# Performance work log

Hardware: AMD Instinct MI355X
Metric: run time of the kernel (lower is better)

The kernel has to match this reference:

```python
import jax, jax.numpy as jnp
import numpy as np

B, N, DEG = 8, 4096, 16
E = N * DEG            # edges per graph
IN, HID, C, OUT = 128, 512, 2, 10
EPS = 1e-15


def setup_inputs() -> dict:
    key = jax.random.key(0)
    ks = jax.random.split(key, 16)
    # within-graph random edges, then offset each graph by b*N
    src = jax.random.randint(ks[0], (B, E), 0, N)
    dst = jax.random.randint(ks[1], (B, E), 0, N)
    off = (jnp.arange(B) * N)[:, None]
    edge_index = jnp.stack([(src + off).reshape(-1), (dst + off).reshape(-1)], axis=0).astype(jnp.int64)
    batch = jnp.repeat(jnp.arange(B), N).astype(jnp.int64)
    x = jax.random.normal(ks[2], (B * N, IN), dtype=jnp.float32)
    edge_weight = jax.random.uniform(ks[3], (B * E,), dtype=jnp.float32)
    g = lambda k, s: (0.02 * jax.random.normal(k, s, dtype=jnp.float32))
    return {
        "x": x, "edge_index": edge_index, "batch": batch, "edge_weight": edge_weight,
        "W_rel1": g(ks[4], (IN, HID)), "b_rel1": jnp.zeros((HID,), jnp.float32),
        "W_root1": g(ks[5], (IN, HID)),
        "W_pool": g(ks[6], (HID, C)), "b_pool": jnp.zeros((C,), jnp.float32),
        "W_rel3": g(ks[7], (HID, HID)), "b_rel3": jnp.zeros((HID,), jnp.float32),
        "W_root3": g(ks[8], (HID, HID)),
        "W_lin1": g(ks[9], (HID, HID)), "b_lin1": jnp.zeros((HID,), jnp.float32),
        "W_lin2": g(ks[10], (HID, OUT)), "b_lin2": jnp.zeros((OUT,), jnp.float32),
    }


def reference(x, edge_index, batch, edge_weight,
              W_rel1, b_rel1, W_root1, W_pool, b_pool,
              W_rel3, b_rel3, W_root3, W_lin1, b_lin1, W_lin2, b_lin2):
    src, dst = edge_index[0], edge_index[1]
    # GraphConv (aggr='add'): out = lin_rel(sum_j w_ji x_j) + lin_root(x)
    agg = jax.ops.segment_sum(x[src] * edge_weight[:, None], dst, num_segments=B * N)
    h = jax.nn.relu(agg @ W_rel1 + b_rel1 + x @ W_root1)          # [BN, HID]
    s_logits = h @ W_pool + b_pool                                 # [BN, C]

    # dense batched tensors (equal-size graphs)
    hd = h.reshape(B, N, HID)
    s = jax.nn.softmax(s_logits.reshape(B, N, C), axis=-1)
    b_idx = batch[src]
    r = src - b_idx * N
    c = dst - b_idx * N
    adj = jnp.zeros((B, N, N), jnp.float32).at[b_idx, r, c].add(edge_weight)

    # dense mincut pooling
    out = jnp.einsum('bnc,bnf->bcf', s, hd)                        # [B, C, HID]
    sA = jnp.einsum('bnc,bnm->bcm', s, adj)
    out_adj = jnp.einsum('bcm,bmk->bck', sA, s)                    # [B, C, C]
    mincut_num = jnp.einsum('bcc->b', out_adj)
    d = adj.sum(-1)                                                # [B, N]
    mincut_den = jnp.einsum('bnc,bn,bnc->b', s, d, s)
    mc_loss = jnp.mean(-(mincut_num / mincut_den))
    ss = jnp.einsum('bnc,bnk->bck', s, s)
    ss_n = ss / jnp.linalg.norm(ss, axis=(1, 2), keepdims=True)
    i_s = jnp.eye(C, dtype=jnp.float32) / jnp.sqrt(jnp.float32(C))
    o_loss = jnp.mean(jnp.linalg.norm(ss_n - i_s[None], axis=(1, 2)))
    # zero diagonal + symmetric degree normalization
    out_adj = out_adj * (1.0 - jnp.eye(C, dtype=jnp.float32))[None]
    d2 = jnp.sqrt(out_adj.sum(-1)) + EPS                           # [B, C]
    out_adj = out_adj / d2[:, :, None] / d2[:, None, :]

    # conv3 on pooled graph: edges (row->col) of dense adj => agg = A^T x
    agg3 = jnp.einsum('bij,bif->bjf', out_adj, out)
    x3 = agg3 @ W_rel3 + b_rel3 + out @ W_root3                    # [B, C, HID]
    xm = x3.mean(axis=1)                                           # [B, HID]
    h2 = jax.nn.relu(xm @ W_lin1 + b_lin1)
    logits = h2 @ W_lin2 + b_lin2
    return (jax.nn.log_softmax(logits, axis=-1), mc_loss, o_loss, s_logits, out_adj)
```

## Files before the change

### kernel.cpp

```cpp
#include <hip/hip_runtime.h>
#include <hip/hip_bf16.h>

#define BB 8
#define NN 4096
#define EE 65536
#define BE (BB*EE)
#define BN (BB*NN)
#define INF 128
#define HID 512
#define CC 2
#define OUTC 10
#define ELLCAP 64

typedef __bf16 bf16x8_t __attribute__((ext_vector_type(8)));
typedef float  f32x4_t  __attribute__((ext_vector_type(4)));

__device__ __forceinline__ ushort f2bf(float f) {
  union { float f; unsigned u; } v; v.f = f;
  unsigned r = v.u + 0x7FFFu + ((v.u >> 16) & 1u);
  return (ushort)(r >> 16);
}
__device__ __forceinline__ float bf2f(ushort s) {
  union { unsigned u; float f; } v; v.u = ((unsigned)s) << 16;
  return v.f;
}

__global__ __launch_bounds__(256) void front(
    const int* __restrict__ src, const int* __restrict__ dst,
    const float* __restrict__ ew, const float* __restrict__ x,
    const float* __restrict__ Wrel, const float* __restrict__ Wroot,
    int* __restrict__ deg, int2* __restrict__ ell,
    ushort* __restrict__ Ab, ushort* __restrict__ Bb) {
  int blk = blockIdx.x;
  int tid = threadIdx.x;
  if (blk < 4096) {
    int g = (blk & 7) * 131072 + (blk >> 3) * 256 + tid;
    float4 v = *(const float4*)&x[(size_t)g * 4];
    int m = g >> 5;
    int kin = (g & 31) * 4;
    ushort4 o;
    o.x = f2bf(v.x); o.y = f2bf(v.y); o.z = f2bf(v.z); o.w = f2bf(v.w);
    *(ushort4*)&Ab[(size_t)m * 256 + 128 + kin] = o;
  } else if (blk < 6144) {
    int bl = blk - 4096;
    int e = (bl & 7) * EE + (bl >> 3) * 256 + tid;
    int d = dst[e];
    int p = atomicAdd(&deg[d], 1);
    if (p < ELLCAP) {
      int2 v; v.x = src[e]; v.y = __float_as_int(ew[e]);
      ell[(size_t)d * ELLCAP + p] = v;
    }
  } else {
    int g = (blk - 6144) * 256 + tid;
    int n = g & 511, k = g >> 9;
    float w = (k < 128) ? Wrel[k * 512 + n] : Wroot[(k - 128) * 512 + n];
    Bb[n * 256 + k] = f2bf(w);
  }
}

__global__ __launch_bounds__(256) void gather_ell(
    const int* __restrict__ deg, const int2* __restrict__ ell,
    ushort* __restrict__ Ab) {
  int blk = blockIdx.x;
  int n = (blk & 7) * NN + (blk >> 3) * 4 + (threadIdx.x >> 6);
  int lane = threadIdx.x & 63;
  int l4 = lane >> 4;
  int fl = lane & 15;
  int d = deg[n]; if (d > ELLCAP) d = ELLCAP;
  const int2* ep = ell + (size_t)n * ELLCAP;

  float a[8] = {0, 0, 0, 0, 0, 0, 0, 0};
  int j = 0;
  for (; j + 7 < d; j += 8) {
    int2 v0 = ep[j + l4];
    int2 v1 = ep[j + 4 + l4];
    uint4 u0 = *(const uint4*)&Ab[(size_t)v0.x * 256 + 128 + fl * 8];
    uint4 u1 = *(const uint4*)&Ab[(size_t)v1.x * 256 + 128 + fl * 8];
    float w0 = __int_as_float(v0.y);
    float w1 = __int_as_float(v1.y);
    const ushort* s0 = (const ushort*)&u0;
    const ushort* s1 = (const ushort*)&u1;
#pragma unroll
    for (int q = 0; q < 8; ++q)
      a[q] += w0 * bf2f(s0[q]) + w1 * bf2f(s1[q]);
  }
  for (; j + 3 < d; j += 4) {
    int2 v0 = ep[j + l4];
    uint4 u0 = *(const uint4*)&Ab[(size_t)v0.x * 256 + 128 + fl * 8];
    float w0 = __int_as_float(v0.y);
    const ushort* s0 = (const ushort*)&u0;
#pragma unroll
    for (int q = 0; q < 8; ++q)
      a[q] += w0 * bf2f(s0[q]);
  }
  {
    int idx = j + l4;
    if (idx < d) {
      int2 v0 = ep[idx];
      uint4 u0 = *(const uint4*)&Ab[(size_t)v0.x * 256 + 128 + fl * 8];
      float w0 = __int_as_float(v0.y);
      const ushort* s0 = (const ushort*)&u0;
#pragma unroll
      for (int q = 0; q < 8; ++q)
        a[q] += w0 * bf2f(s0[q]);
    }
  }
#pragma unroll
  for (int q = 0; q < 8; ++q) {
    a[q] += __shfl_xor(a[q], 16, 64);
    a[q] += __shfl_xor(a[q], 32, 64);
  }
  if (l4 == 0) {
    ushort o[8];
#pragma unroll
    for (int q = 0; q < 8; ++q) o[q] = f2bf(a[q]);
    *(uint4*)&Ab[(size_t)n * 256 + fl * 8] = *(const uint4*)o;
  }
}

#define CPAD 72
__global__ __launch_bounds__(256) void gemm_mfma(
    const ushort* __restrict__ Ab, const ushort* __restrict__ Bb,
    const float* __restrict__ brel, ushort* __restrict__ hw) {
  __shared__ ushort As[64 * 256];
  __shared__ ushort Bs[64 * 256];
  int tid = threadIdx.x;
  int blk = blockIdx.x;
  int xcd = blk & 7;
  int idx = blk >> 3;
  int by = xcd * 64 + (idx & 63);
  int bx = idx >> 6;
  int m0 = by * 64, n0 = bx * 64;

#pragma unroll
  for (int i = 0; i < 8; ++i) {
    int g = tid + i * 256;
    int r = g >> 5, c = g & 31;
    int cs = c ^ (r & 31);
    *(uint4*)&As[(r * 32 + cs) * 8] = *(const uint4*)&Ab[(size_t)(m0 + r) * 256 + c * 8];
    *(uint4*)&Bs[(r * 32 + cs) * 8] = *(const uint4*)&Bb[(size_t)(n0 + r) * 256 + c * 8];
  }
  __syncthreads();

  int wave = tid >> 6, lane = tid & 63;
  int wm = (wave >> 1) * 32, wn = (wave & 1) * 32;
  int l16 = lane & 15, quad = lane >> 4;

  f32x4_t acc[2][2];
#pragma unroll
  for (int f = 0; f < 2; ++f)
#pragma unroll
    for (int g = 0; g < 2; ++g) acc[f][g] = (f32x4_t){0.f, 0.f, 0.f, 0.f};

  int arow[2] = {wm + l16, wm + 16 + l16};
  int brow[2] = {wn + l16, wn + 16 + l16};

#pragma unroll
  for (int kc = 0; kc < 8; ++kc) {
    int cl = kc * 4 + quad;
    bf16x8_t af[2], bf[2];
#pragma unroll
    for (int f = 0; f < 2; ++f) {
      af[f] = *(const bf16x8_t*)&As[(arow[f] * 32 + (cl ^ (arow[f] & 31))) * 8];
      bf[f] = *(const bf16x8_t*)&Bs[(brow[f] * 32 + (cl ^ (brow[f] & 31))) * 8];
    }
#pragma unroll
    for (int f = 0; f < 2; ++f)
#pragma unroll
      for (int g = 0; g < 2; ++g)
        acc[f][g] = __builtin_amdgcn_mfma_f32_16x16x32_bf16(af[f], bf[g], acc[f][g], 0, 0, 0);
  }
  __syncthreads();

  ushort* Cs = As;
#pragma unroll
  for (int g = 0; g < 2; ++g) {
    int col = wn + g * 16 + l16;
    float bias = brel[n0 + col];
#pragma unroll
    for (int f = 0; f < 2; ++f) {
      int rowb = wm + f * 16 + quad * 4;
#pragma unroll
      for (int r = 0; r < 4; ++r) {
        float v = fmaxf(acc[f][g][r] + bias, 0.f);
        Cs[(rowb + r) * CPAD + col] = f2bf(v);
      }
    }
  }
  __syncthreads();
  {
    int r = tid >> 2, co = (tid & 3) * 16;
    uint4 v0 = *(uint4*)&Cs[r * CPAD + co];
    uint4 v1 = *(uint4*)&Cs[r * CPAD + co + 8];
    *(uint4*)&hw[(size_t)(m0 + r) * 512 + n0 + co] = v0;
    *(uint4*)&hw[(size_t)(m0 + r) * 512 + n0 + co + 8] = v1;
  }
}

__global__ __launch_bounds__(256) void pool_node(
    const ushort* __restrict__ hw, const float* __restrict__ Wp,
    const float* __restrict__ bp, float* __restrict__ s,
    float* __restrict__ slog, float* __restrict__ outpart,
    float* __restrict__ ssacc) {
  __shared__ float red[4][1024];
  __shared__ float ssr[4][3];
  int blk = blockIdx.x;
  int b = blk & 7;
  int chunk = blk >> 3;
  int obik = b * 64 + chunk;
  int wave = threadIdx.x >> 6, lane = threadIdx.x & 63;
  int n0 = b * NN + chunk * 64 + wave * 16;
  int f0 = lane * 8;

  float wp0[8], wp1[8];
#pragma unroll
  for (int j = 0; j < 8; ++j) {
    wp0[j] = Wp[(f0 + j) * 2];
    wp1[j] = Wp[(f0 + j) * 2 + 1];
  }
  float bp0 = bp[0], bp1 = bp[1];
  float o0[8] = {0, 0, 0, 0, 0, 0, 0, 0};
  float o1[8] = {0, 0, 0, 0, 0, 0, 0, 0};
  float sa = 0.f, sb = 0.f, sc2 = 0.f;

  for (int i = 0; i < 16; ++i) {
    int n = n0 + i;
    bf16x8_t hv = *(const bf16x8_t*)&hw[(size_t)n * HID + f0];
    const ushort* hp = (const ushort*)&hv;
    float h[8];
    float a0 = 0.f, a1 = 0.f;
#pragma unroll
    for (int j = 0; j < 8; ++j) {
      h[j] = bf2f(hp[j]);
      a0 += h[j] * wp0[j];
      a1 += h[j] * wp1[j];
    }
#pragma unroll
    for (int off = 32; off; off >>= 1) {
      a0 += __shfl_down(a0, off, 64);
      a1 += __shfl_down(a1, off, 64);
    }
    float s0 = 0.f, s1 = 0.f;
    if (lane == 0) {
      float l0 = a0 + bp0, l1 = a1 + bp1;
      slog[n * 2] = l0;
      slog[n * 2 + 1] = l1;
      float m = fmaxf(l0, l1);
      float e0 = expf(l0 - m), e1 = expf(l1 - m);
      float inv = 1.f / (e0 + e1);
      s0 = e0 * inv; s1 = e1 * inv;
      s[n * 2] = s0;
      s[n * 2 + 1] = s1;
      sa += s0 * s0; sb += s0 * s1; sc2 += s1 * s1;
    }
    s0 = __shfl(s0, 0, 64);
    s1 = __shfl(s1, 0, 64);
#pragma unroll
    for (int j = 0; j < 8; ++j) {
      o0[j] += s0 * h[j];
      o1[j] += s1 * h[j];
    }
  }

#pragma unroll
  for (int j = 0; j < 8; ++j) {
    red[wave][f0 + j] = o0[j];
    red[wave][512 + f0 + j] = o1[j];
  }
  if (lane == 0) { ssr[wave][0] = sa; ssr[wave][1] = sb; ssr[wave][2] = sc2; }
  __syncthreads();
  int t = threadIdx.x;
#pragma unroll
  for (int q = 0; q < 4; ++q) {
    int idx = t + q * 256;
    float v = red[0][idx] + red[1][idx] + red[2][idx] + red[3][idx];
    outpart[(size_t)obik * 1024 + idx] = v;
  }
  if (t < 3) {
    float v = ssr[0][t] + ssr[1][t] + ssr[2][t] + ssr[3][t];
    atomicAdd(&ssacc[b * 4 + t], v);
  }
}

__global__ __launch_bounds__(256) void edge_pass2(
    const int* __restrict__ src, const int* __restrict__ dst,
    const float* __restrict__ ew, const float* __restrict__ s,
    float* __restrict__ oadj, float* __restrict__ mden) {
  int b = blockIdx.x & 7;
  int sub = blockIdx.x >> 3;
  int base = b * EE + sub * 1024;
  float p00 = 0, p01 = 0, p10 = 0, p11 = 0, md = 0;
  for (int i = threadIdx.x; i < 1024; i += 256) {
    int e = base + i;
    int r = src[e], c = dst[e];
    float w = ew[e];
    float s0r = s[r * 2], s1r = s[r * 2 + 1];
    float s0c = s[c * 2], s1c = s[c * 2 + 1];
    p00 += w * s0r * s0c; p01 += w * s0r * s1c;
    p10 += w * s1r * s0c; p11 += w * s1r * s1c;
    md  += w * (s0r * s0r + s1r * s1r);
  }
#pragma unroll
  for (int off = 32; off; off >>= 1) {
    p00 += __shfl_down(p00, off, 64);
    p01 += __shfl_down(p01, off, 64);
    p10 += __shfl_down(p10, off, 64);
    p11 += __shfl_down(p11, off, 64);
    md  += __shfl_down(md,  off, 64);
  }
  __shared__ float red[4][5];
  int wave = threadIdx.x >> 6, lane = threadIdx.x & 63;
  if (lane == 0) {
    red[wave][0] = p00; red[wave][1] = p01;
    red[wave][2] = p10; red[wave][3] = p11;
    red[wave][4] = md;
  }
  __syncthreads();
  if (threadIdx.x < 4) {
    float v = red[0][threadIdx.x] + red[1][threadIdx.x] +
              red[2][threadIdx.x] + red[3][threadIdx.x];
    atomicAdd(&oadj[b * 4 + threadIdx.x], v);
  } else if (threadIdx.x == 4) {
    float v = red[0][4] + red[1][4] + red[2][4] + red[3][4];
    atomicAdd(&mden[b], v);
  }
}

__global__ __launch_bounds__(256) void finalize_a(
    const float* __restrict__ outpart, const float* __restrict__ oadj,
    const float* __restrict__ ssacc, const float* __restrict__ mden,
    float* __restrict__ uv, float* __restrict__ lossp,
    float* __restrict__ dout) {
  __shared__ float sc[2];
  int b = blockIdx.x, t = threadIdx.x;
  if (t == 0) {
    float r00 = oadj[b * 4 + 0], r01 = oadj[b * 4 + 1];
    float r10 = oadj[b * 4 + 2], r11 = oadj[b * 4 + 3];
    lossp[b * 2 + 0] = -((r00 + r11) / mden[b]) / (float)BB;
    float a = ssacc[b * 4 + 0], bb = ssacc[b * 4 + 1], c = ssacc[b * 4 + 2];
    float nrm = sqrtf(a * a + 2.f * bb * bb + c * c);
    float q = 0.70710678118654752f;
    float da = a / nrm - q, db = bb / nrm, dc = c / nrm - q;
    lossp[b * 2 + 1] = sqrtf(da * da + 2.f * db * db + dc * dc) / (float)BB;
    float d20 = sqrtf(r01) + 1e-15f;
    float d21 = sqrtf(r10) + 1e-15f;
    float oa01 = r01 / (d20 * d21);
    float oa10 = r10 / (d21 * d20);
    dout[65618 + b * 4 + 0] = 0.f;
    dout[65618 + b * 4 + 1] = oa01;
    dout[65618 + b * 4 + 2] = oa10;
    dout[65618 + b * 4 + 3] = 0.f;
    sc[0] = oa01; sc[1] = oa10;
  }
  __syncthreads();
  float oa01 = sc[0], oa10 = sc[1];
  for (int f = t; f < HID; f += 256) {
    float o0 = 0.f, o1 = 0.f;
    for (int i = 0; i < 64; ++i) {
      o0 += outpart[(size_t)(b * 64 + i) * 1024 + f];
      o1 += outpart[(size_t)(b * 64 + i) * 1024 + 512 + f];
    }
    uv[b * HID + f] = oa10 * o1 + oa01 * o0;
    uv[BB * HID + b * HID + f] = o0 + o1;
  }
}

__global__ __launch_bounds__(256) void conv3_part(
    const float* __restrict__ uv, const float* __restrict__ Wrel3,
    const float* __restrict__ Wroot3, float* __restrict__ xmacc) {
  __shared__ float us[8][32], vs[8][32];
  __shared__ float red[4][64][8];
  int blk = blockIdx.x;
  int fc = blk & 7, kc = blk >> 3;
  int t = threadIdx.x;
  {
    int b = t >> 5, k = t & 31;
    us[b][k] = uv[b * HID + kc * 32 + k];
    vs[b][k] = uv[BB * HID + b * HID + kc * 32 + k];
  }
  __syncthreads();
  int f = fc * 64 + (t & 63);
  int ks = t >> 6;
  float acc[8] = {0, 0, 0, 0, 0, 0, 0, 0};
#pragma unroll
  for (int j = 0; j < 8; ++j) {
    int kl = ks * 8 + j;
    int k = kc * 32 + kl;
    float wr = Wrel3[k * HID + f];
    float wo = Wroot3[k * HID + f];
#pragma unroll
    for (int b = 0; b < 8; ++b)
      acc[b] += us[b][kl] * wr + vs[b][kl] * wo;
  }
#pragma unroll
  for (int b = 0; b < 8; ++b) red[ks][t & 63][b] = acc[b];
  __syncthreads();
  if (ks == 0) {
    int fl = t & 63;
#pragma unroll
    for (int b = 0; b < 8; ++b) {
      float v = red[0][fl][b] + red[1][fl][b] + red[2][fl][b] + red[3][fl][b];
      atomicAdd(&xmacc[b * HID + f], v);
    }
  }
}

__global__ __launch_bounds__(256) void lin1_part(
    const float* __restrict__ xmacc, const float* __restrict__ brel3,
    const float* __restrict__ Wlin1, float* __restrict__ h2acc) {
  __shared__ float xs[8][32];
  __shared__ float red[4][64][8];
  int blk = blockIdx.x;
  int fc = blk & 7, kc = blk >> 3;
  int t = threadIdx.x;
  {
    int b = t >> 5, k = t & 31;
    xs[b][k] = 0.5f * xmacc[b * HID + kc * 32 + k] + brel3[kc * 32 + k];
  }
  __syncthreads();
  int f = fc * 64 + (t & 63);
  int ks = t >> 6;
  float acc[8] = {0, 0, 0, 0, 0, 0, 0, 0};
#pragma unroll
  for (int j = 0; j < 8; ++j) {
    int kl = ks * 8 + j;
    int k = kc * 32 + kl;
    float w = Wlin1[k * HID + f];
#pragma unroll
    for (int b = 0; b < 8; ++b)
      acc[b] += xs[b][kl] * w;
  }
#pragma unroll
  for (int b = 0; b < 8; ++b) red[ks][t & 63][b] = acc[b];
  __syncthreads();
  if (ks == 0) {
    int fl = t & 63;
#pragma unroll
    for (int b = 0; b < 8; ++b) {
      float v = red[0][fl][b] + red[1][fl][b] + red[2][fl][b] + red[3][fl][b];
      atomicAdd(&h2acc[b * HID + f], v);
    }
  }
}

__global__ __launch_bounds__(256) void head(
    const float* __restrict__ h2acc, const float* __restrict__ blin1,
    const float* __restrict__ Wlin2, const float* __restrict__ blin2,
    const float* __restrict__ lossp, float* __restrict__ dout) {
  __shared__ float hs[HID];
  __shared__ float lg[16];
  __shared__ float lse;
  int b = blockIdx.x, t = threadIdx.x;
  if (b == 0 && t == 255) {
    float l0 = 0.f, l1 = 0.f;
#pragma unroll
    for (int i = 0; i < BB; ++i) { l0 += lossp[i * 2]; l1 += lossp[i * 2 + 1]; }
    dout[80] = l0;
    dout[81] = l1;
  }
  for (int i = t; i < HID; i += 256)
    hs[i] = fmaxf(h2acc[b * HID + i] + blin1[i], 0.f);
  __syncthreads();
  int wave = t >> 6, lane = t & 63;
  for (int o = wave; o < OUTC; o += 4) {
    float acc = 0.f;
    for (int k = lane; k < HID; k += 64)
      acc += hs[k] * Wlin2[k * OUTC + o];
#pragma unroll
    for (int off = 32; off; off >>= 1) acc += __shfl_down(acc, off, 64);
    if (lane == 0) lg[o] = acc + blin2[o];
  }
  __syncthreads();
  if (t == 0) {
    float m = lg[0];
    for (int o = 1; o < OUTC; ++o) m = fmaxf(m, lg[o]);
    float se = 0.f;
    for (int o = 0; o < OUTC; ++o) se += expf(lg[o] - m);
    lse = m + logf(se);
  }
  __syncthreads();
  if (t < OUTC) dout[b * OUTC + t] = lg[t] - lse;
}

extern "C" void kernel_launch(void* const* d_in, const int* in_sizes, int n_in,
                              void* d_out, int out_size, void* d_ws, size_t ws_size,
                              hipStream_t stream) {
  const float* x      = (const float*)d_in[0];
  const int*   ei     = (const int*)d_in[1];
  const float* ew     = (const float*)d_in[3];
  const float* Wrel1  = (const float*)d_in[4];
  const float* brel1  = (const float*)d_in[5];
  const float* Wroot1 = (const float*)d_in[6];
  const float* Wpool  = (const float*)d_in[7];
  const float* bpool  = (const float*)d_in[8];
  const float* Wrel3  = (const float*)d_in[9];
  const float* brel3  = (const float*)d_in[10];
  const float* Wroot3 = (const float*)d_in[11];
  const float* Wlin1  = (const float*)d_in[12];
  const float* blin1  = (const float*)d_in[13];
  const float* Wlin2  = (const float*)d_in[14];
  const float* blin2  = (const float*)d_in[15];
  float* out = (float*)d_out;
  float* ws  = (float*)d_ws;

  float* oadj  = ws + 40960;
  float* ssacc = oadj + 32;
  float* mden  = ssacc + 32;
  int*   deg   = (int*)(mden + 8);
  float* xmacc = ws + 73800;
  float* h2acc = xmacc + 4096;
  float* lossp = ws + 81992;
  ushort* Ab   = (ushort*)(ws + 106568);
  ushort* Bb   = (ushort*)(ws + 4300872);
  ushort* hbf  = (ushort*)(ws + 4366408);
  float* outpart = ws + 12763208;
  int2*  ell   = (int2*)(ws + 4366408);
  float* s     = ws + 106568;
  float* uv    = (float*)deg;

  const int* src = ei;
  const int* dst = ei + BE;

  hipMemsetAsync(ws + 40960, 0, (size_t)41032 * sizeof(float), stream);

  front      <<<6656, 256, 0, stream>>>(src, dst, ew, x, Wrel1, Wroot1,
                                        deg, ell, Ab, Bb);
  gather_ell <<<BN / 4, 256, 0, stream>>>(deg, ell, Ab);
  gemm_mfma  <<<4096, 256, 0, stream>>>(Ab, Bb, brel1, hbf);
  pool_node  <<<512, 256, 0, stream>>>(hbf, Wpool, bpool, s, out + 82, outpart, ssacc);
  edge_pass2 <<<BB * 64, 256, 0, stream>>>(src, dst, ew, s, oadj, mden);
  finalize_a <<<BB, 256, 0, stream>>>(outpart, oadj, ssacc, mden, uv, lossp, out);
  conv3_part <<<128, 256, 0, stream>>>(uv, Wrel3, Wroot3, xmacc);
  lin1_part  <<<128, 256, 0, stream>>>(xmacc, brel3, Wlin1, h2acc);
  head       <<<BB, 256, 0, stream>>>(h2acc, blin1, Wlin2, blin2, lossp, out);
}
```

Baseline: 218.3 us.

## Fuse conv1 GEMM with pooling so h stays in LDS; split finalize_a

```diff
diff --git a/kernel.cpp b/kernel.cpp
--- a/kernel.cpp
+++ b/kernel.cpp
@@ -118,19 +118,22 @@
   }
 }
 
-#define CPAD 72
-__global__ __launch_bounds__(256) void gemm_mfma(
+__global__ __launch_bounds__(256) void gemm_pool(
     const ushort* __restrict__ Ab, const ushort* __restrict__ Bb,
-    const float* __restrict__ brel, ushort* __restrict__ hw) {
+    const float* __restrict__ brel, const float* __restrict__ Wp,
+    const float* __restrict__ bp, float* __restrict__ s,
+    float* __restrict__ slog, float* __restrict__ outpart,
+    float* __restrict__ ssacc) {
   __shared__ ushort As[64 * 256];
   __shared__ ushort Bs[64 * 256];
+  __shared__ ushort hS[64 * 512];
+  __shared__ float ssr[4][3];
   int tid = threadIdx.x;
   int blk = blockIdx.x;
-  int xcd = blk & 7;
-  int idx = blk >> 3;
-  int by = xcd * 64 + (idx & 63);
-  int bx = idx >> 6;
-  int m0 = by * 64, n0 = bx * 64;
+  int b = blk & 7;
+  int chunk = blk >> 3;
+  int m0 = b * NN + chunk * 64;
+  int obik = b * 64 + chunk;
 
 #pragma unroll
   for (int i = 0; i < 8; ++i) {
@@ -138,80 +141,51 @@
     int r = g >> 5, c = g & 31;
     int cs = c ^ (r & 31);
     *(uint4*)&As[(r * 32 + cs) * 8] = *(const uint4*)&Ab[(size_t)(m0 + r) * 256 + c * 8];
-    *(uint4*)&Bs[(r * 32 + cs) * 8] = *(const uint4*)&Bb[(size_t)(n0 + r) * 256 + c * 8];
-  }
-  __syncthreads();
+  }
 
   int wave = tid >> 6, lane = tid & 63;
-  int wm = (wave >> 1) * 32, wn = (wave & 1) * 32;
+  int wm = wave * 16;
   int l16 = lane & 15, quad = lane >> 4;
-
-  f32x4_t acc[2][2];
-#pragma unroll
-  for (int f = 0; f < 2; ++f)
-#pragma unroll
-    for (int g = 0; g < 2; ++g) acc[f][g] = (f32x4_t){0.f, 0.f, 0.f, 0.f};
-
-  int arow[2] = {wm + l16, wm + 16 + l16};
-  int brow[2] = {wn + l16, wn + 16 + l16};
-
-#pragma unroll
-  for (int kc = 0; kc < 8; ++kc) {
-    int cl = kc * 4 + quad;
-    bf16x8_t af[2], bf[2];
-#pragma unroll
-    for (int f = 0; f < 2; ++f) {
-      af[f] = *(const bf16x8_t*)&As[(arow[f] * 32 + (cl ^ (arow[f] & 31))) * 8];
-      bf[f] = *(const bf16x8_t*)&Bs[(brow[f] * 32 + (cl ^ (brow[f] & 31))) * 8];
-    }
-#pragma unroll
-    for (int f = 0; f < 2; ++f)
-#pragma unroll
-      for (int g = 0; g < 2; ++g)
-        acc[f][g] = __builtin_amdgcn_mfma_f32_16x16x32_bf16(af[f], bf[g], acc[f][g], 0, 0, 0);
-  }
-  __syncthreads();
-
-  ushort* Cs = As;
-#pragma unroll
-  for (int g = 0; g < 2; ++g) {
-    int col = wn + g * 16 + l16;
-    float bias = brel[n0 + col];
-#pragma unroll
-    for (int f = 0; f < 2; ++f) {
-      int rowb = wm + f * 16 + quad * 4;
-#pragma unroll
-      for (int r = 0; r < 4; ++r) {
-        float v = fmaxf(acc[f][g][r] + bias, 0.f);
-        Cs[(rowb + r) * CPAD + col] = f2bf(v);
+  int arow = wm + l16;
+
+  for (int cc = 0; cc < 8; ++cc) {
+    int n0 = cc * 64;
+#pragma unroll
+    for (int i = 0; i < 8; ++i) {
+      int g = tid + i * 256;
+      int r = g >> 5, c = g & 31;
+      int cs = c ^ (r & 31);
+      *(uint4*)&Bs[(r * 32 + cs) * 8] = *(const uint4*)&Bb[(size_t)(n0 + r) * 256 + c * 8];
+    }
+    __syncthreads();
+
+    f32x4_t acc[4];
+#pragma unroll
+    for (int ct = 0; ct < 4; ++ct) acc[ct] = (f32x4_t){0.f, 0.f, 0.f, 0.f};
+#pragma unroll
+    for (int kc = 0; kc < 8; ++kc) {
+      int cl = kc * 4 + quad;
+      bf16x8_t af = *(const bf16x8_t*)&As[(arow * 32 + (cl ^ (arow & 31))) * 8];
+#pragma unroll
+      for (int ct = 0; ct < 4; ++ct) {
+        int brow = ct * 16 + l16;
+        bf16x8_t bf = *(const bf16x8_t*)&Bs[(brow * 32 + (cl ^ (brow & 31))) * 8];
+        acc[ct] = __builtin_amdgcn_mfma_f32_16x16x32_bf16(af, bf, acc[ct], 0, 0, 0);
       }
     }
-  }
-  __syncthreads();
-  {
-    int r = tid >> 2, co = (tid & 3) * 16;
-    uint4 v0 = *(uint4*)&Cs[r * CPAD + co];
-    uint4 v1 = *(uint4*)&Cs[r * CPAD + co + 8];
-    *(uint4*)&hw[(size_t)(m0 + r) * 512 + n0 + co] = v0;
-    *(uint4*)&hw[(size_t)(m0 + r) * 512 + n0 + co + 8] = v1;
-  }
-}
-
-__global__ __launch_bounds__(256) void pool_node(
-    const ushort* __restrict__ hw, const float* __restrict__ Wp,
-    const float* __restrict__ bp, float* __restrict__ s,
-    float* __restrict__ slog, float* __restrict__ outpart,
-    float* __restrict__ ssacc) {
-  __shared__ float red[4][1024];
-  __shared__ float ssr[4][3];
-  int blk = blockIdx.x;
-  int b = blk & 7;
-  int chunk = blk >> 3;
-  int obik = b * 64 + chunk;
-  int wave = threadIdx.x >> 6, lane = threadIdx.x & 63;
-  int n0 = b * NN + chunk * 64 + wave * 16;
+#pragma unroll
+    for (int ct = 0; ct < 4; ++ct) {
+      int col = n0 + ct * 16 + l16;
+      float bias = brel[col];
+      int rowb = wm + quad * 4;
+#pragma unroll
+      for (int r = 0; r < 4; ++r)
+        hS[(rowb + r) * 512 + col] = f2bf(fmaxf(acc[ct][r] + bias, 0.f));
+    }
+    __syncthreads();
+  }
+
   int f0 = lane * 8;
-
   float wp0[8], wp1[8];
 #pragma unroll
   for (int j = 0; j < 8; ++j) {
@@ -224,8 +198,9 @@
   float sa = 0.f, sb = 0.f, sc2 = 0.f;
 
   for (int i = 0; i < 16; ++i) {
-    int n = n0 + i;
-    bf16x8_t hv = *(const bf16x8_t*)&hw[(size_t)n * HID + f0];
+    int nl = wm + i;
+    int n = m0 + nl;
+    bf16x8_t hv = *(const bf16x8_t*)&hS[(size_t)nl * 512 + f0];
     const ushort* hp = (const ushort*)&hv;
     float h[8];
     float a0 = 0.f, a1 = 0.f;
@@ -262,23 +237,23 @@
     }
   }
 
+  float* red = (float*)As;
 #pragma unroll
   for (int j = 0; j < 8; ++j) {
-    red[wave][f0 + j] = o0[j];
-    red[wave][512 + f0 + j] = o1[j];
+    red[wave * 1024 + f0 + j] = o0[j];
+    red[wave * 1024 + 512 + f0 + j] = o1[j];
   }
   if (lane == 0) { ssr[wave][0] = sa; ssr[wave][1] = sb; ssr[wave][2] = sc2; }
   __syncthreads();
-  int t = threadIdx.x;
 #pragma unroll
   for (int q = 0; q < 4; ++q) {
-    int idx = t + q * 256;
-    float v = red[0][idx] + red[1][idx] + red[2][idx] + red[3][idx];
+    int idx = tid + q * 256;
+    float v = red[idx] + red[1024 + idx] + red[2048 + idx] + red[3072 + idx];
     outpart[(size_t)obik * 1024 + idx] = v;
   }
-  if (t < 3) {
-    float v = ssr[0][t] + ssr[1][t] + ssr[2][t] + ssr[3][t];
-    atomicAdd(&ssacc[b * 4 + t], v);
+  if (tid < 3) {
+    float v = ssr[0][tid] + ssr[1][tid] + ssr[2][tid] + ssr[3][tid];
+    atomicAdd(&ssacc[b * 4 + tid], v);
   }
 }
 
@@ -332,36 +307,47 @@
     float* __restrict__ uv, float* __restrict__ lossp,
     float* __restrict__ dout) {
   __shared__ float sc[2];
-  int b = blockIdx.x, t = threadIdx.x;
+  __shared__ float r0[256], r1[256];
+  int b = blockIdx.x >> 3, fc = blockIdx.x & 7;
+  int t = threadIdx.x;
   if (t == 0) {
     float r00 = oadj[b * 4 + 0], r01 = oadj[b * 4 + 1];
     float r10 = oadj[b * 4 + 2], r11 = oadj[b * 4 + 3];
-    lossp[b * 2 + 0] = -((r00 + r11) / mden[b]) / (float)BB;
-    float a = ssacc[b * 4 + 0], bb = ssacc[b * 4 + 1], c = ssacc[b * 4 + 2];
-    float nrm = sqrtf(a * a + 2.f * bb * bb + c * c);
-    float q = 0.70710678118654752f;
-    float da = a / nrm - q, db = bb / nrm, dc = c / nrm - q;
-    lossp[b * 2 + 1] = sqrtf(da * da + 2.f * db * db + dc * dc) / (float)BB;
     float d20 = sqrtf(r01) + 1e-15f;
     float d21 = sqrtf(r10) + 1e-15f;
     float oa01 = r01 / (d20 * d21);
     float oa10 = r10 / (d21 * d20);
-    dout[65618 + b * 4 + 0] = 0.f;
-    dout[65618 + b * 4 + 1] = oa01;
-    dout[65618 + b * 4 + 2] = oa10;
-    dout[65618 + b * 4 + 3] = 0.f;
     sc[0] = oa01; sc[1] = oa10;
-  }
-  __syncthreads();
-  float oa01 = sc[0], oa10 = sc[1];
-  for (int f = t; f < HID; f += 256) {
-    float o0 = 0.f, o1 = 0.f;
-    for (int i = 0; i < 64; ++i) {
-      o0 += outpart[(size_t)(b * 64 + i) * 1024 + f];
-      o1 += outpart[(size_t)(b * 64 + i) * 1024 + 512 + f];
-    }
-    uv[b * HID + f] = oa10 * o1 + oa01 * o0;
-    uv[BB * HID + b * HID + f] = o0 + o1;
+    if (fc == 0) {
+      lossp[b * 2 + 0] = -((r00 + r11) / mden[b]) / (float)BB;
+      float a = ssacc[b * 4 + 0], bb = ssacc[b * 4 + 1], c = ssacc[b * 4 + 2];
+      float nrm = sqrtf(a * a + 2.f * bb * bb + c * c);
+      float q = 0.70710678118654752f;
+      float da = a / nrm - q, db = bb / nrm, dc = c / nrm - q;
+      lossp[b * 2 + 1] = sqrtf(da * da + 2.f * db * db + dc * dc) / (float)BB;
+      dout[65618 + b * 4 + 0] = 0.f;
+      dout[65618 + b * 4 + 1] = oa01;
+      dout[65618 + b * 4 + 2] = oa10;
+      dout[65618 + b * 4 + 3] = 0.f;
+    }
+  }
+  __syncthreads();
+  int f = fc * 64 + (t & 63);
+  int ic = t >> 6;
+  float o0s = 0.f, o1s = 0.f;
+  for (int i = ic * 16; i < ic * 16 + 16; ++i) {
+    o0s += outpart[(size_t)(b * 64 + i) * 1024 + f];
+    o1s += outpart[(size_t)(b * 64 + i) * 1024 + 512 + f];
+  }
+  r0[ic * 64 + (t & 63)] = o0s;
+  r1[ic * 64 + (t & 63)] = o1s;
+  __syncthreads();
+  if (ic == 0) {
+    int fl = t & 63;
+    float a0 = r0[fl] + r0[64 + fl] + r0[128 + fl] + r0[192 + fl];
+    float a1 = r1[fl] + r1[64 + fl] + r1[128 + fl] + r1[192 + fl];
+    uv[b * HID + f] = sc[1] * a1 + sc[0] * a0;
+    uv[BB * HID + b * HID + f] = a0 + a1;
   }
 }
 
@@ -512,10 +498,9 @@
   float* lossp = ws + 81992;
   ushort* Ab   = (ushort*)(ws + 106568);
   ushort* Bb   = (ushort*)(ws + 4300872);
-  ushort* hbf  = (ushort*)(ws + 4366408);
   float* outpart = ws + 12763208;
+  float* s     = ws + 16000000;
   int2*  ell   = (int2*)(ws + 4366408);
-  float* s     = ws + 106568;
   float* uv    = (float*)deg;
 
   const int* src = ei;
@@ -526,10 +511,10 @@
   front      <<<6656, 256, 0, stream>>>(src, dst, ew, x, Wrel1, Wroot1,
                                         deg, ell, Ab, Bb);
   gather_ell <<<BN / 4, 256, 0, stream>>>(deg, ell, Ab);
-  gemm_mfma  <<<4096, 256, 0, stream>>>(Ab, Bb, brel1, hbf);
-  pool_node  <<<512, 256, 0, stream>>>(hbf, Wpool, bpool, s, out + 82, outpart, ssacc);
+  gemm_pool  <<<512, 256, 0, stream>>>(Ab, Bb, brel1, Wpool, bpool,
+                                       s, out + 82, outpart, ssacc);
   edge_pass2 <<<BB * 64, 256, 0, stream>>>(src, dst, ew, s, oadj, mden);
-  finalize_a <<<BB, 256, 0, stream>>>(outpart, oadj, ssacc, mden, uv, lossp, out);
+  finalize_a <<<64, 256, 0, stream>>>(outpart, oadj, ssacc, mden, uv, lossp, out);
   conv3_part <<<128, 256, 0, stream>>>(uv, Wrel3, Wroot3, xmacc);
   lin1_part  <<<128, 256, 0, stream>>>(xmacc, brel3, Wlin1, h2acc);
   head       <<<BB, 256, 0, stream>>>(h2acc, blin1, Wlin2, blin2, lossp, out);
```

Measured after the change: 209.7 us. -4.0%, faster.
